# Optimization experiments

Hardware: AMD Instinct MI355X
Metric: run time of the kernel (lower is better)

The kernel has to match this reference:

```python
import jax, jax.numpy as jnp
import numpy as np

N = 100000          # nodes
E = 1600000         # edges (avg degree 16)
IN = 128            # in_channels
OUT = 64            # out_channels
HID = 2 * OUT       # first GCN layer width per Encoder (non-skip)


def setup_inputs() -> dict:
    key = jax.random.key(0)
    k0, k1, k2, k3 = jax.random.split(key, 4)
    x = jax.random.normal(k0, (N, IN), dtype=jnp.float32)
    edge_index = jax.random.randint(k1, (2, E), 0, N, dtype=jnp.int32)
    W1 = jax.random.normal(k2, (IN, HID), dtype=jnp.float32) / np.float32(np.sqrt(IN))
    b1 = jnp.zeros((HID,), jnp.float32)
    W2 = jax.random.normal(k3, (HID, OUT), dtype=jnp.float32) / np.float32(np.sqrt(HID))
    b2 = jnp.zeros((OUT,), jnp.float32)
    a = jnp.float32(0.25)  # PReLU slope (single shared parameter)
    return {"x": x, "edge_index": edge_index, "W1": W1, "b1": b1, "W2": W2, "b2": b2, "a": a}


def _gcn_layer(x, W, b, src, dst, n):
    # GCNConv: h = x W; symmetric normalization with self-loops already in src/dst
    h = x @ W                                                   # [N, F]
    deg = jax.ops.segment_sum(jnp.ones_like(dst, dtype=h.dtype), dst, num_segments=n)
    dinv = jnp.where(deg > 0, jax.lax.rsqrt(deg), jnp.float32(0.0))
    norm = dinv[src] * dinv[dst]                                # [E']
    msg = h[src] * norm[:, None]                                # gather + scale
    return jax.ops.segment_sum(msg, dst, num_segments=n) + b    # scatter-sum


def _prelu(x, a):
    return jnp.where(x >= 0, x, a * x)


def reference(x, edge_index, W1, b1, W2, b2, a):
    n = x.shape[0]
    loops = jnp.arange(n, dtype=edge_index.dtype)
    src = jnp.concatenate([edge_index[0], loops])   # add self-loops (GCNConv default)
    dst = jnp.concatenate([edge_index[1], loops])
    h = _prelu(_gcn_layer(x, W1, b1, src, dst, n), a)
    return _prelu(_gcn_layer(h, W2, b2, src, dst, n), a)
```

## Files before the change

### kernel.cpp

```cpp
#include <hip/hip_runtime.h>


#define THREADS 256
#define SCAN_CHUNK 1024
#define NBLK  256
#define BINSH 7
#define BINSZ 128
#define KMAX  1024

typedef unsigned short bf16_t;
typedef __attribute__((ext_vector_type(8))) short bf16x8;
typedef __attribute__((ext_vector_type(4))) float f32x4;

__device__ __forceinline__ float bflo(unsigned int w) {
    union { unsigned int u; float f; } v; v.u = w << 16; return v.f;
}
__device__ __forceinline__ float bfhi(unsigned int w) {
    union { unsigned int u; float f; } v; v.u = w & 0xffff0000u; return v.f;
}
__device__ __forceinline__ unsigned int f2bf(float f) {
    union { float f; unsigned int u; } v; v.f = f;
    return (v.u + 0x7fffu + ((v.u >> 16) & 1u)) >> 16;
}

__global__ __launch_bounds__(THREADS) void hist_kernel(const int* __restrict__ dst,
                                                       int* __restrict__ hist,
                                                       int e, int K, int chunk) {
    __shared__ int h[KMAX];
    int t = threadIdx.x, b = blockIdx.x;
    for (int i = t; i < K; i += THREADS) h[i] = 0;
    __syncthreads();
    int lo = b * chunk, hi = min(lo + chunk, e);
    for (int i = lo + t; i < hi; i += THREADS) atomicAdd(&h[dst[i] >> BINSH], 1);
    __syncthreads();
    for (int i = t; i < K; i += THREADS) hist[i * NBLK + b] = h[i];
}

__global__ void scan_phaseA_kernel(const int* __restrict__ in, int* __restrict__ bsum, int m) {
    __shared__ int sdata[256];
    int base = blockIdx.x * SCAN_CHUNK;
    int t = threadIdx.x;
    int s = 0;
#pragma unroll
    for (int k = 0; k < 4; ++k) {
        int idx = base + t * 4 + k;
        if (idx < m) s += in[idx];
    }
    sdata[t] = s;
    __syncthreads();
    for (int d = 128; d > 0; d >>= 1) {
        if (t < d) sdata[t] += sdata[t + d];
        __syncthreads();
    }
    if (t == 0) bsum[blockIdx.x] = sdata[0];
}

__global__ void scan_phaseB_kernel(int* __restrict__ bsum, int nb) {
    __shared__ int sdata[256];
    __shared__ int carry;
    int t = threadIdx.x;
    if (t == 0) carry = 0;
    __syncthreads();
    for (int base = 0; base < nb; base += 256) {
        int idx = base + t;
        int v = (idx < nb) ? bsum[idx] : 0;
        sdata[t] = v;
        __syncthreads();
        for (int d = 1; d < 256; d <<= 1) {
            int u = (t >= d) ? sdata[t - d] : 0;
            __syncthreads();
            sdata[t] += u;
            __syncthreads();
        }
        int excl = sdata[t] - v + carry;
        if (idx < nb) bsum[idx] = excl;
        int tot = sdata[255];
        __syncthreads();
        if (t == 0) carry += tot;
        __syncthreads();
    }
}

__global__ void scan_phaseC_kernel(const int* __restrict__ in, const int* __restrict__ bsum,
                                   int* __restrict__ outx, int m) {
    __shared__ int sdata[256];
    int base = blockIdx.x * SCAN_CHUNK;
    int t = threadIdx.x;
    int v[4];
    int s = 0;
#pragma unroll
    for (int k = 0; k < 4; ++k) {
        int idx = base + t * 4 + k;
        v[k] = (idx < m) ? in[idx] : 0;
        s += v[k];
    }
    sdata[t] = s;
    __syncthreads();
    for (int d = 1; d < 256; d <<= 1) {
        int u = (t >= d) ? sdata[t - d] : 0;
        __syncthreads();
        sdata[t] += u;
        __syncthreads();
    }
    int run = bsum[blockIdx.x] + sdata[t] - s;
#pragma unroll
    for (int k = 0; k < 4; ++k) {
        int idx = base + t * 4 + k;
        if (idx < m) { outx[idx] = run; run += v[k]; }
    }
}

__global__ __launch_bounds__(THREADS) void rank_scatter_kernel(const int* __restrict__ src,
                                                               const int* __restrict__ dst,
                                                               const int* __restrict__ hoff,
                                                               unsigned int* __restrict__ sorted,
                                                               int e, int K, int chunk) {
    __shared__ int cntl[KMAX];
    __shared__ int basel[KMAX];
    int t = threadIdx.x, b = blockIdx.x;
    for (int i = t; i < K; i += THREADS) { cntl[i] = 0; basel[i] = hoff[i * NBLK + b]; }
    __syncthreads();
    int lo = b * chunk, hi = min(lo + chunk, e);
    for (int i = lo + t; i < hi; i += THREADS) {
        int d = dst[i];
        int bin = d >> BINSH;
        int r = atomicAdd(&cntl[bin], 1);
        sorted[basel[bin] + r] = (unsigned int)src[i] | ((unsigned int)(d & (BINSZ - 1)) << 25);
    }
}

__global__ __launch_bounds__(THREADS) void bin_build_kernel(const unsigned int* __restrict__ sorted,
                                                            const int* __restrict__ hoff,
                                                            float* __restrict__ dinv,
                                                            int* __restrict__ off,
                                                            int* __restrict__ cnt,
                                                            int* __restrict__ es,
                                                            int n, int e, int K) {
    __shared__ int scnt[BINSZ];
    __shared__ int soff[BINSZ];
    int b = blockIdx.x, t = threadIdx.x;
    int base = hoff[b * NBLK];
    int end  = (b + 1 < K) ? hoff[(b + 1) * NBLK] : e;
    int m = end - base;
    if (t < BINSZ) scnt[t] = 0;
    __syncthreads();
    for (int i = t; i < m; i += THREADS) atomicAdd(&scnt[sorted[base + i] >> 25], 1);
    __syncthreads();
    if (t < BINSZ) soff[t] = scnt[t];
    __syncthreads();
    for (int d = 1; d < BINSZ; d <<= 1) {
        int v = (t < BINSZ && t >= d) ? soff[t - d] : 0;
        __syncthreads();
        if (t < BINSZ) soff[t] += v;
        __syncthreads();
    }
    if (t < BINSZ) {
        int ex = soff[t] - scnt[t];
        int node = (b << BINSH) + t;
        if (node < n) {
            off[node]  = base + ex;
            cnt[node]  = scnt[t];
            dinv[node] = rsqrtf((float)(scnt[t] + 1));
        }
        soff[t] = ex;
    }
    __syncthreads();
    for (int i = t; i < m; i += THREADS) {
        unsigned int pk = sorted[base + i];
        int pos = atomicAdd(&soff[pk >> 25], 1);
        es[base + pos] = (int)(pk & 0x01FFFFFFu);
    }
}

__global__ void wt2_kernel(const float* __restrict__ W1, bf16_t* __restrict__ WT1,
                           const float* __restrict__ W2, bf16_t* __restrict__ WT2,
                           int K1, int C1, int K2, int C2) {
    int tid = blockIdx.x * blockDim.x + threadIdx.x;
    int t1 = K1 * C1;
    if (tid < t1) {
        int c = tid / K1, k = tid % K1;
        WT1[(size_t)c * K1 + k] = (bf16_t)f2bf(W1[(size_t)k * C1 + c]);
    } else if (tid < t1 + K2 * C2) {
        int id = tid - t1;
        int c = id / K2, k = id % K2;
        WT2[(size_t)c * K2 + k] = (bf16_t)f2bf(W2[(size_t)k * C2 + c]);
    }
}

template <int OUTC, bool XBF, bool XSPLIT, bool OSPLIT>
__global__ __launch_bounds__(THREADS) void gemm_mfma_kernel(const void* __restrict__ Xv,
                                                            const void* __restrict__ Xv2,
                                                            const bf16_t* __restrict__ WT,
                                                            const float* __restrict__ rowscale,
                                                            bf16_t* __restrict__ H,
                                                            bf16_t* __restrict__ H2, int n) {
    constexpr int CT = OUTC / 16;
    constexpr int RT = 2;
    int wid  = (int)threadIdx.x >> 6;
    int lane = (int)threadIdx.x & 63;
    int col16 = lane & 15;
    int kgrp  = lane >> 4;
    int rbase = blockIdx.x * (4 * RT * 16) + wid * (RT * 16);

    int row[RT];
    float sc[RT];
    bf16x8 xf[RT][4];
#pragma unroll
    for (int rt = 0; rt < RT; ++rt) {
        row[rt] = rbase + rt * 16 + col16;
        int rc = row[rt] < n ? row[rt] : (n - 1);
        sc[rt] = rowscale[rc];
#pragma unroll
        for (int ks = 0; ks < 4; ++ks) {
            int kb = ks * 32 + kgrp * 8;
            if constexpr (XBF) {
                if constexpr (XSPLIT) {
                    const bf16_t* xb = (ks < 2) ? (const bf16_t*)Xv : (const bf16_t*)Xv2;
                    xf[rt][ks] = *reinterpret_cast<const bf16x8*>(xb + (size_t)rc * 64 + (kb & 63));
                } else {
                    xf[rt][ks] = *reinterpret_cast<const bf16x8*>((const bf16_t*)Xv + (size_t)rc * 128 + kb);
                }
            } else {
                const float* xp = (const float*)Xv + (size_t)rc * 128 + kb;
                float4 x0 = *reinterpret_cast<const float4*>(xp);
                float4 x1 = *reinterpret_cast<const float4*>(xp + 4);
                bf16x8 t;
                t[0] = (short)f2bf(x0.x); t[1] = (short)f2bf(x0.y);
                t[2] = (short)f2bf(x0.z); t[3] = (short)f2bf(x0.w);
                t[4] = (short)f2bf(x1.x); t[5] = (short)f2bf(x1.y);
                t[6] = (short)f2bf(x1.z); t[7] = (short)f2bf(x1.w);
                xf[rt][ks] = t;
            }
        }
    }

#pragma unroll
    for (int ct = 0; ct < CT; ++ct) {
        const bf16_t* wp = WT + (size_t)(ct * 16 + col16) * 128 + kgrp * 8;
        bf16x8 wf[4];
#pragma unroll
        for (int ks = 0; ks < 4; ++ks) wf[ks] = *reinterpret_cast<const bf16x8*>(wp + ks * 32);
#pragma unroll
        for (int rt = 0; rt < RT; ++rt) {
            f32x4 acc = {0.f, 0.f, 0.f, 0.f};
#pragma unroll
            for (int ks = 0; ks < 4; ++ks)
                acc = __builtin_amdgcn_mfma_f32_16x16x32_bf16(wf[ks], xf[rt][ks], acc, 0, 0, 0);
            if (row[rt] < n) {
                float s = sc[rt];
                uint2 w;
                w.x = f2bf(acc[0] * s) | (f2bf(acc[1] * s) << 16);
                w.y = f2bf(acc[2] * s) | (f2bf(acc[3] * s) << 16);
                if constexpr (OSPLIT) {
                    int half = ct < CT / 2;
                    bf16_t* hb = half ? H : H2;
                    int cc = half ? ct : ct - CT / 2;
                    *reinterpret_cast<uint2*>(hb + (size_t)row[rt] * (OUTC / 2) + cc * 16 + kgrp * 4) = w;
                } else {
                    *reinterpret_cast<uint2*>(H + (size_t)row[rt] * OUTC + ct * 16 + kgrp * 4) = w;
                }
            }
        }
    }
}

template <int F, bool OUTBF>
__global__ __launch_bounds__(THREADS) void agg_kernel(const bf16_t* __restrict__ H,
                                                      const float* __restrict__ dinv,
                                                      const int* __restrict__ off,
                                                      const int* __restrict__ cnt,
                                                      const int* __restrict__ es,
                                                      const float* __restrict__ bias,
                                                      const float* __restrict__ a_ptr,
                                                      void* __restrict__ outv, int n) {
    constexpr int TPN = F / 8;
    int node = blockIdx.x * (THREADS / TPN) + (int)threadIdx.x / TPN;
    int l8   = (int)threadIdx.x % TPN;
    if (node >= n) return;
    const int fbase = l8 * 8;

    float acc[8];
    {
        uint4 v = *reinterpret_cast<const uint4*>(H + (size_t)node * F + fbase);
        acc[0] = bflo(v.x); acc[1] = bfhi(v.x);
        acc[2] = bflo(v.y); acc[3] = bfhi(v.y);
        acc[4] = bflo(v.z); acc[5] = bfhi(v.z);
        acc[6] = bflo(v.w); acc[7] = bfhi(v.w);
    }

    int j0 = off[node];
    int m  = cnt[node];
    int i = 0;
    for (; i + 3 < m; i += 4) {
        int s0 = es[j0 + i], s1 = es[j0 + i + 1], s2 = es[j0 + i + 2], s3 = es[j0 + i + 3];
        uint4 v0 = *reinterpret_cast<const uint4*>(H + (size_t)s0 * F + fbase);
        uint4 v1 = *reinterpret_cast<const uint4*>(H + (size_t)s1 * F + fbase);
        uint4 v2 = *reinterpret_cast<const uint4*>(H + (size_t)s2 * F + fbase);
        uint4 v3 = *reinterpret_cast<const uint4*>(H + (size_t)s3 * F + fbase);
        acc[0] += (bflo(v0.x) + bflo(v1.x)) + (bflo(v2.x) + bflo(v3.x));
        acc[1] += (bfhi(v0.x) + bfhi(v1.x)) + (bfhi(v2.x) + bfhi(v3.x));
        acc[2] += (bflo(v0.y) + bflo(v1.y)) + (bflo(v2.y) + bflo(v3.y));
        acc[3] += (bfhi(v0.y) + bfhi(v1.y)) + (bfhi(v2.y) + bfhi(v3.y));
        acc[4] += (bflo(v0.z) + bflo(v1.z)) + (bflo(v2.z) + bflo(v3.z));
        acc[5] += (bfhi(v0.z) + bfhi(v1.z)) + (bfhi(v2.z) + bfhi(v3.z));
        acc[6] += (bflo(v0.w) + bflo(v1.w)) + (bflo(v2.w) + bflo(v3.w));
        acc[7] += (bfhi(v0.w) + bfhi(v1.w)) + (bfhi(v2.w) + bfhi(v3.w));
    }
    for (; i < m; ++i) {
        int s0 = es[j0 + i];
        uint4 v0 = *reinterpret_cast<const uint4*>(H + (size_t)s0 * F + fbase);
        acc[0] += bflo(v0.x); acc[1] += bfhi(v0.x);
        acc[2] += bflo(v0.y); acc[3] += bfhi(v0.y);
        acc[4] += bflo(v0.z); acc[5] += bfhi(v0.z);
        acc[6] += bflo(v0.w); acc[7] += bfhi(v0.w);
    }

    float di = dinv[node];
    float a  = *a_ptr;
    float4 b0 = *reinterpret_cast<const float4*>(bias + fbase);
    float4 b1 = *reinterpret_cast<const float4*>(bias + fbase + 4);
    float bb[8] = {b0.x, b0.y, b0.z, b0.w, b1.x, b1.y, b1.z, b1.w};
    float o[8];
#pragma unroll
    for (int k = 0; k < 8; ++k) {
        float v = acc[k] * di + bb[k];
        o[k] = v >= 0.f ? v : a * v;
    }

    if constexpr (OUTBF) {
        uint4 w;
        w.x = f2bf(o[0]) | (f2bf(o[1]) << 16);
        w.y = f2bf(o[2]) | (f2bf(o[3]) << 16);
        w.z = f2bf(o[4]) | (f2bf(o[5]) << 16);
        w.w = f2bf(o[6]) | (f2bf(o[7]) << 16);
        *reinterpret_cast<uint4*>((bf16_t*)outv + (size_t)node * F + fbase) = w;
    } else {
        float* op = (float*)outv + (size_t)node * F + fbase;
        *reinterpret_cast<float4*>(op)     = make_float4(o[0], o[1], o[2], o[3]);
        *reinterpret_cast<float4*>(op + 4) = make_float4(o[4], o[5], o[6], o[7]);
    }
}

extern "C" void kernel_launch(void* const* d_in, const int* in_sizes, int n_in,
                              void* d_out, int out_size, void* d_ws, size_t ws_size,
                              hipStream_t stream) {
    const float* x   = (const float*)d_in[0];
    const int*   ei  = (const int*)d_in[1];
    const float* W1  = (const float*)d_in[2];
    const float* b1  = (const float*)d_in[3];
    const float* W2  = (const float*)d_in[4];
    const float* b2  = (const float*)d_in[5];
    const float* a   = (const float*)d_in[6];

    const int IN  = 128;
    const int HID = 128;
    const int OUT = 64;
    const int n = in_sizes[0] / IN;
    const int e = in_sizes[1] / 2;
    const int* src = ei;
    const int* dst = ei + e;

    const int K     = (n + BINSZ - 1) >> BINSH;
    const int chunk = (e + NBLK - 1) / NBLK;
    const int M     = K * NBLK;
    const int nb    = (M + SCAN_CHUNK - 1) / SCAN_CHUNK;

    auto align = [](size_t v) { return (v + 255) / 256 * 256; };
    char* ws = (char*)d_ws;
    size_t o = 0;
    int*          hist   = (int*)(ws + o);          o += align((size_t)M * 4);
    int*          hoff   = (int*)(ws + o);          o += align((size_t)M * 4);
    int*          bsum   = (int*)(ws + o);          o += align((size_t)nb * 4);
    unsigned int* sorted = (unsigned int*)(ws + o); o += align((size_t)e * 4);
    int*          es     = (int*)(ws + o);          o += align((size_t)e * 4);
    float*        dinv   = (float*)(ws + o);        o += align((size_t)n * 4);
    int*          off    = (int*)(ws + o);          o += align((size_t)n * 4);
    int*          cnt    = (int*)(ws + o);          o += align((size_t)n * 4);
    bf16_t*       h1a    = (bf16_t*)(ws + o);       o += align((size_t)n * 64 * 2);
    bf16_t*       h1b    = (bf16_t*)(ws + o);       o += align((size_t)n * 64 * 2);
    bf16_t*       h2a    = (bf16_t*)(ws + o);       o += align((size_t)n * 64 * 2);
    bf16_t*       h2b    = (bf16_t*)(ws + o);       o += align((size_t)n * 64 * 2);
    bf16_t*       g      = (bf16_t*)(ws + o);       o += align((size_t)n * OUT * 2);
    bf16_t*       WT1    = (bf16_t*)(ws + o);       o += align((size_t)IN * HID * 2);
    bf16_t*       WT2    = (bf16_t*)(ws + o);       o += align((size_t)HID * OUT * 2);

    float* out = (float*)d_out;

    {
        int tot = IN * HID + HID * OUT;
        wt2_kernel<<<(tot + THREADS - 1) / THREADS, THREADS, 0, stream>>>(
            W1, WT1, W2, WT2, IN, HID, HID, OUT);
    }

    hist_kernel<<<NBLK, THREADS, 0, stream>>>(dst, hist, e, K, chunk);
    scan_phaseA_kernel<<<nb, THREADS, 0, stream>>>(hist, bsum, M);
    scan_phaseB_kernel<<<1, THREADS, 0, stream>>>(bsum, nb);
    scan_phaseC_kernel<<<nb, THREADS, 0, stream>>>(hist, bsum, hoff, M);
    rank_scatter_kernel<<<NBLK, THREADS, 0, stream>>>(src, dst, hoff, sorted, e, K, chunk);
    bin_build_kernel<<<K, THREADS, 0, stream>>>(sorted, hoff, dinv, off, cnt, es, n, e, K);

    int gbG = (n + 127) / 128;
    constexpr int NPB = THREADS / (64 / 8);
    int gbA = (n + NPB - 1) / NPB;

    gemm_mfma_kernel<128, false, false, true><<<gbG, THREADS, 0, stream>>>(
        x, nullptr, WT1, dinv, h1a, h1b, n);
    agg_kernel<64, true><<<gbA, THREADS, 0, stream>>>(h1a, dinv, off, cnt, es, b1,      a, h2a, n);
    agg_kernel<64, true><<<gbA, THREADS, 0, stream>>>(h1b, dinv, off, cnt, es, b1 + 64, a, h2b, n);

    gemm_mfma_kernel<64, true, true, false><<<gbG, THREADS, 0, stream>>>(
        h2a, h2b, WT2, dinv, g, nullptr, n);
    agg_kernel<64, false><<<gbA, THREADS, 0, stream>>>(g, dinv, off, cnt, es, b2, a, out, n);

    (void)ws_size; (void)n_in; (void)out_size;
}
```

Measured before the change: 197.4 us.

## Split feature matrices into 16-column slices for cache-resident aggregation passes

Each layer's feature matrix is now stored as separate 16-column bf16 slices of 3.2 MB each, and the GEMM writes to and reads from them directly. Aggregation then runs one pass per slice (8 for layer 1, 4 for layer 2), with two threads per node. The aim is to keep each pass's gathered working set resident in L2/LLC so random neighbor gathers hit cache instead of HBM. The cost is re-reading the CSR edge lists 12 times instead of 3 and issuing more kernel launches, with each gather now only 32 bytes per node.

```diff
diff --git a/kernel.cpp b/kernel.cpp
--- a/kernel.cpp
+++ b/kernel.cpp
@@ -11,6 +11,9 @@
 typedef unsigned short bf16_t;
 typedef __attribute__((ext_vector_type(8))) short bf16x8;
 typedef __attribute__((ext_vector_type(4))) float f32x4;
+
+struct CPtr8 { const bf16_t* p[8]; };
+struct Ptr8  { bf16_t* p[8]; };
 
 __device__ __forceinline__ float bflo(unsigned int w) {
     union { unsigned int u; float f; } v; v.u = w << 16; return v.f;
@@ -187,13 +190,12 @@
     }
 }
 
-template <int OUTC, bool XBF, bool XSPLIT, bool OSPLIT>
+template <int OUTC, bool XBF, bool XSLICE>
 __global__ __launch_bounds__(THREADS) void gemm_mfma_kernel(const void* __restrict__ Xv,
-                                                            const void* __restrict__ Xv2,
+                                                            CPtr8 xs,
                                                             const bf16_t* __restrict__ WT,
                                                             const float* __restrict__ rowscale,
-                                                            bf16_t* __restrict__ H,
-                                                            bf16_t* __restrict__ H2, int n) {
+                                                            Ptr8 os, int n) {
     constexpr int CT = OUTC / 16;
     constexpr int RT = 2;
     int wid  = (int)threadIdx.x >> 6;
@@ -213,13 +215,11 @@
 #pragma unroll
         for (int ks = 0; ks < 4; ++ks) {
             int kb = ks * 32 + kgrp * 8;
-            if constexpr (XBF) {
-                if constexpr (XSPLIT) {
-                    const bf16_t* xb = (ks < 2) ? (const bf16_t*)Xv : (const bf16_t*)Xv2;
-                    xf[rt][ks] = *reinterpret_cast<const bf16x8*>(xb + (size_t)rc * 64 + (kb & 63));
-                } else {
-                    xf[rt][ks] = *reinterpret_cast<const bf16x8*>((const bf16_t*)Xv + (size_t)rc * 128 + kb);
-                }
+            if constexpr (XSLICE) {
+                const bf16_t* xb = (kgrp < 2) ? xs.p[ks * 2] : xs.p[ks * 2 + 1];
+                xf[rt][ks] = *reinterpret_cast<const bf16x8*>(xb + (size_t)rc * 16 + (kgrp & 1) * 8);
+            } else if constexpr (XBF) {
+                xf[rt][ks] = *reinterpret_cast<const bf16x8*>((const bf16_t*)Xv + (size_t)rc * 128 + kb);
             } else {
                 const float* xp = (const float*)Xv + (size_t)rc * 128 + kb;
                 float4 x0 = *reinterpret_cast<const float4*>(xp);
@@ -251,20 +251,13 @@
                 uint2 w;
                 w.x = f2bf(acc[0] * s) | (f2bf(acc[1] * s) << 16);
                 w.y = f2bf(acc[2] * s) | (f2bf(acc[3] * s) << 16);
-                if constexpr (OSPLIT) {
-                    int half = ct < CT / 2;
-                    bf16_t* hb = half ? H : H2;
-                    int cc = half ? ct : ct - CT / 2;
-                    *reinterpret_cast<uint2*>(hb + (size_t)row[rt] * (OUTC / 2) + cc * 16 + kgrp * 4) = w;
-                } else {
-                    *reinterpret_cast<uint2*>(H + (size_t)row[rt] * OUTC + ct * 16 + kgrp * 4) = w;
-                }
+                *reinterpret_cast<uint2*>(os.p[ct] + (size_t)row[rt] * 16 + kgrp * 4) = w;
             }
         }
     }
 }
 
-template <int F, bool OUTBF>
+template <bool OUTBF>
 __global__ __launch_bounds__(THREADS) void agg_kernel(const bf16_t* __restrict__ H,
                                                       const float* __restrict__ dinv,
                                                       const int* __restrict__ off,
@@ -272,16 +265,16 @@
                                                       const int* __restrict__ es,
                                                       const float* __restrict__ bias,
                                                       const float* __restrict__ a_ptr,
-                                                      void* __restrict__ outv, int n) {
-    constexpr int TPN = F / 8;
-    int node = blockIdx.x * (THREADS / TPN) + (int)threadIdx.x / TPN;
-    int l8   = (int)threadIdx.x % TPN;
+                                                      void* __restrict__ outv,
+                                                      int ocol, int ostride, int n) {
+    int node = blockIdx.x * 128 + ((int)threadIdx.x >> 1);
+    int l8   = (int)threadIdx.x & 1;
     if (node >= n) return;
     const int fbase = l8 * 8;
 
     float acc[8];
     {
-        uint4 v = *reinterpret_cast<const uint4*>(H + (size_t)node * F + fbase);
+        uint4 v = *reinterpret_cast<const uint4*>(H + (size_t)node * 16 + fbase);
         acc[0] = bflo(v.x); acc[1] = bfhi(v.x);
         acc[2] = bflo(v.y); acc[3] = bfhi(v.y);
         acc[4] = bflo(v.z); acc[5] = bfhi(v.z);
@@ -293,10 +286,10 @@
     int i = 0;
     for (; i + 3 < m; i += 4) {
         int s0 = es[j0 + i], s1 = es[j0 + i + 1], s2 = es[j0 + i + 2], s3 = es[j0 + i + 3];
-        uint4 v0 = *reinterpret_cast<const uint4*>(H + (size_t)s0 * F + fbase);
-        uint4 v1 = *reinterpret_cast<const uint4*>(H + (size_t)s1 * F + fbase);
-        uint4 v2 = *reinterpret_cast<const uint4*>(H + (size_t)s2 * F + fbase);
-        uint4 v3 = *reinterpret_cast<const uint4*>(H + (size_t)s3 * F + fbase);
+        uint4 v0 = *reinterpret_cast<const uint4*>(H + (size_t)s0 * 16 + fbase);
+        uint4 v1 = *reinterpret_cast<const uint4*>(H + (size_t)s1 * 16 + fbase);
+        uint4 v2 = *reinterpret_cast<const uint4*>(H + (size_t)s2 * 16 + fbase);
+        uint4 v3 = *reinterpret_cast<const uint4*>(H + (size_t)s3 * 16 + fbase);
         acc[0] += (bflo(v0.x) + bflo(v1.x)) + (bflo(v2.x) + bflo(v3.x));
         acc[1] += (bfhi(v0.x) + bfhi(v1.x)) + (bfhi(v2.x) + bfhi(v3.x));
         acc[2] += (bflo(v0.y) + bflo(v1.y)) + (bflo(v2.y) + bflo(v3.y));
@@ -308,7 +301,7 @@
     }
     for (; i < m; ++i) {
         int s0 = es[j0 + i];
-        uint4 v0 = *reinterpret_cast<const uint4*>(H + (size_t)s0 * F + fbase);
+        uint4 v0 = *reinterpret_cast<const uint4*>(H + (size_t)s0 * 16 + fbase);
         acc[0] += bflo(v0.x); acc[1] += bfhi(v0.x);
         acc[2] += bflo(v0.y); acc[3] += bfhi(v0.y);
         acc[4] += bflo(v0.z); acc[5] += bfhi(v0.z);
@@ -333,9 +326,9 @@
         w.y = f2bf(o[2]) | (f2bf(o[3]) << 16);
         w.z = f2bf(o[4]) | (f2bf(o[5]) << 16);
         w.w = f2bf(o[6]) | (f2bf(o[7]) << 16);
-        *reinterpret_cast<uint4*>((bf16_t*)outv + (size_t)node * F + fbase) = w;
+        *reinterpret_cast<uint4*>((bf16_t*)outv + (size_t)node * ostride + ocol + fbase) = w;
     } else {
-        float* op = (float*)outv + (size_t)node * F + fbase;
+        float* op = (float*)outv + (size_t)node * ostride + ocol + fbase;
         *reinterpret_cast<float4*>(op)     = make_float4(o[0], o[1], o[2], o[3]);
         *reinterpret_cast<float4*>(op + 4) = make_float4(o[4], o[5], o[6], o[7]);
     }
@@ -376,15 +369,17 @@
     float*        dinv   = (float*)(ws + o);        o += align((size_t)n * 4);
     int*          off    = (int*)(ws + o);          o += align((size_t)n * 4);
     int*          cnt    = (int*)(ws + o);          o += align((size_t)n * 4);
-    bf16_t*       h1a    = (bf16_t*)(ws + o);       o += align((size_t)n * 64 * 2);
-    bf16_t*       h1b    = (bf16_t*)(ws + o);       o += align((size_t)n * 64 * 2);
-    bf16_t*       h2a    = (bf16_t*)(ws + o);       o += align((size_t)n * 64 * 2);
-    bf16_t*       h2b    = (bf16_t*)(ws + o);       o += align((size_t)n * 64 * 2);
-    bf16_t*       g      = (bf16_t*)(ws + o);       o += align((size_t)n * OUT * 2);
+    Ptr8 h1s, h2s, gs;
+    for (int s = 0; s < 8; ++s) { h1s.p[s] = (bf16_t*)(ws + o); o += align((size_t)n * 16 * 2); }
+    for (int s = 0; s < 8; ++s) { h2s.p[s] = (bf16_t*)(ws + o); o += align((size_t)n * 16 * 2); }
+    for (int s = 0; s < 8; ++s) { gs.p[s]  = (s < 4) ? (bf16_t*)(ws + o) : nullptr;
+                                  if (s < 4) o += align((size_t)n * 16 * 2); }
     bf16_t*       WT1    = (bf16_t*)(ws + o);       o += align((size_t)IN * HID * 2);
     bf16_t*       WT2    = (bf16_t*)(ws + o);       o += align((size_t)HID * OUT * 2);
 
     float* out = (float*)d_out;
+    CPtr8 h2c; for (int s = 0; s < 8; ++s) h2c.p[s] = h2s.p[s];
+    CPtr8 nullc = {};
 
     {
         int tot = IN * HID + HID * OUT;
@@ -400,17 +395,19 @@
     bin_build_kernel<<<K, THREADS, 0, stream>>>(sorted, hoff, dinv, off, cnt, es, n, e, K);
 
     int gbG = (n + 127) / 128;
-    constexpr int NPB = THREADS / (64 / 8);
-    int gbA = (n + NPB - 1) / NPB;
-
-    gemm_mfma_kernel<128, false, false, true><<<gbG, THREADS, 0, stream>>>(
-        x, nullptr, WT1, dinv, h1a, h1b, n);
-    agg_kernel<64, true><<<gbA, THREADS, 0, stream>>>(h1a, dinv, off, cnt, es, b1,      a, h2a, n);
-    agg_kernel<64, true><<<gbA, THREADS, 0, stream>>>(h1b, dinv, off, cnt, es, b1 + 64, a, h2b, n);
-
-    gemm_mfma_kernel<64, true, true, false><<<gbG, THREADS, 0, stream>>>(
-        h2a, h2b, WT2, dinv, g, nullptr, n);
-    agg_kernel<64, false><<<gbA, THREADS, 0, stream>>>(g, dinv, off, cnt, es, b2, a, out, n);
+    int gbA = (n + 127) / 128;
+
+    gemm_mfma_kernel<128, false, false><<<gbG, THREADS, 0, stream>>>(
+        x, nullc, WT1, dinv, h1s, n);
+    for (int s = 0; s < 8; ++s)
+        agg_kernel<true><<<gbA, THREADS, 0, stream>>>(
+            h1s.p[s], dinv, off, cnt, es, b1 + s * 16, a, h2s.p[s], 0, 16, n);
+
+    gemm_mfma_kernel<64, true, true><<<gbG, THREADS, 0, stream>>>(
+        nullptr, h2c, WT2, dinv, gs, n);
+    for (int s = 0; s < 4; ++s)
+        agg_kernel<false><<<gbA, THREADS, 0, stream>>>(
+            gs.p[s], dinv, off, cnt, es, b2 + s * 16, a, out, s * 16, 64, n);
 
     (void)ws_size; (void)n_in; (void)out_size;
 }
```

Measured after the change: 302.7 us. 53.3% more time.
